# Optimization experiments

Measured on AMD Instinct MI355X. Metric: run time of the kernel, lower is better.

Reference implementation:

```python
import jax, jax.numpy as jnp
import numpy as np

B, N, Y, C = 8, 512, 64, 256


def setup_inputs() -> dict:
    key = jax.random.key(0)
    ks = jax.random.split(key, 7)
    sampled = jax.random.normal(ks[0], (B, N, Y, C), dtype=jnp.float32)
    # binary visibility mask (original passes 0/1-ish validity)
    valid = jnp.round(jax.random.uniform(ks[1], (B, N, Y), dtype=jnp.float32))
    # buffer: normalized y depth steps, y_steps = arange(Y)
    y_steps = jnp.arange(Y, dtype=jnp.float32)
    y_norm = (y_steps - y_steps.min()) / jnp.maximum(y_steps.max() - y_steps.min(), 1e-6)
    # weight_mlp = Linear(C+1 -> C), GELU, Linear(C -> 1); store weights pre-transposed (in, out)
    s1 = 1.0 / np.sqrt(C + 1)
    s2 = 1.0 / np.sqrt(C)
    W1 = jax.random.uniform(ks[2], (C + 1, C), dtype=jnp.float32, minval=-s1, maxval=s1)
    b1 = jax.random.uniform(ks[3], (C,), dtype=jnp.float32, minval=-s1, maxval=s1)
    W2 = jax.random.uniform(ks[4], (C, 1), dtype=jnp.float32, minval=-s2, maxval=s2)
    b2 = jax.random.uniform(ks[5], (1,), dtype=jnp.float32, minval=-s2, maxval=s2)
    return {"sampled": sampled, "valid": valid, "y_norm": y_norm,
            "W1": W1, "b1": b1, "W2": W2, "b2": b2}


def reference(sampled, valid, y_norm, W1, b1, W2, b2):
    b, n, y, c = sampled.shape
    yfeat = jnp.broadcast_to(y_norm.reshape(1, 1, y, 1), (b, n, y, 1))
    feat = jnp.concatenate([sampled, yfeat], axis=-1)            # [B,N,Y,C+1]
    h = jax.nn.gelu(feat @ W1 + b1, approximate=False)            # [B,N,Y,C]
    logits = (h @ W2 + b2)[..., 0]                                # [B,N,Y]
    logits = jnp.where(valid < 0.5, jnp.float32(-10000.0), logits)
    weights = jax.nn.softmax(logits, axis=-1) * valid
    denom = jnp.maximum(weights.sum(axis=-1, keepdims=True), 1e-6)
    weights = weights / denom
    return jnp.einsum('bnyc,bny->bnc', sampled, weights)          # [B,N,C]
```

## Files before the change

kernel.cpp:

```cpp
#include <hip/hip_runtime.h>

#define NTOK 4096
#define AST  264

using short8  = __attribute__((ext_vector_type(8))) short;
using short4v = __attribute__((ext_vector_type(4))) short;
using floatx4 = __attribute__((ext_vector_type(4))) float;

static __device__ __forceinline__ short f2bf(float f) {
  union { float f; unsigned u; } v; v.f = f;
  unsigned u = v.u;
  u = (u + 0x7fffu + ((u >> 16) & 1u)) >> 16;
  return (short)u;
}

static __device__ __forceinline__ float bf2f(short s) {
  union { unsigned u; float f; } v; v.u = ((unsigned)(unsigned short)s) << 16;
  return v.f;
}

static __device__ __forceinline__ float fast_gelu(float z) {
  float x  = z * 0.70710678118654752f;
  float ax = fabsf(x);
  float t  = __builtin_amdgcn_rcpf(fmaf(0.3275911f, ax, 1.0f));
  float em = __expf(-ax * ax);
  float p  = fmaf(fmaf(fmaf(fmaf(1.061405429f, t, -1.453152027f), t,
                            1.421413741f), t, -0.284496736f), t, 0.254829592f);
  float er = fmaf(-p * t, em, 1.0f);
  unsigned sgn = __float_as_uint(x) & 0x80000000u;
  er = __uint_as_float(__float_as_uint(er) | sgn);
  return z * fmaf(0.5f, er, 0.5f);
}

__global__ void prep_w1(const float* __restrict__ W1, short* __restrict__ W1s) {
  const int n  = threadIdx.x;
  const int kb = blockIdx.x;
  const int s  = kb >> 2;
  const int l  = ((kb & 3) << 4) | (n & 15);
  const int t  = n >> 4;
  short8 o;
  #pragma unroll
  for (int j = 0; j < 8; ++j)
    o[j] = f2bf(W1[(kb * 8 + j) * 256 + n]);
  *(short8*)(W1s + (((s * 16 + t) * 64 + l) << 3)) = o;
}

__global__ void __launch_bounds__(256, 4) agg_kernel(
    const float* __restrict__ sampled, const float* __restrict__ valid,
    const float* __restrict__ y_norm, const float* __restrict__ W1,
    const float* __restrict__ b1, const float* __restrict__ W2,
    const float* __restrict__ b2, const short* __restrict__ W1s,
    float* __restrict__ out) {
  __shared__ __align__(16) short Abf[64 * AST];
  __shared__ float wlog[4][64];
  __shared__ float ynl[64];

  const int tid = threadIdx.x;
  const int tok = blockIdx.x;
  const float* S = sampled + ((size_t)tok << 14);

  if (tid < 64) ynl[tid] = y_norm[tid];
  const float4* S4 = (const float4*)S;
  #pragma unroll
  for (int h = 0; h < 2; ++h) {
    float4 v[8];
    #pragma unroll
    for (int it = 0; it < 8; ++it) v[it] = S4[(h * 8 + it) * 256 + tid];
    #pragma unroll
    for (int it = 0; it < 8; ++it) {
      int j  = (h * 8 + it) * 256 + tid;
      int y  = j >> 6;
      int k4 = (j & 63) << 2;
      short4v p;
      p[0] = f2bf(v[it].x); p[1] = f2bf(v[it].y);
      p[2] = f2bf(v[it].z); p[3] = f2bf(v[it].w);
      *(short4v*)(&Abf[y * AST + k4]) = p;
    }
  }
  __syncthreads();

  const int wv  = tid >> 6;
  const int ln  = tid & 63;
  const int q   = ln >> 4;
  const int c15 = ln & 15;

  const floatx4 fzero = {0.f, 0.f, 0.f, 0.f};
  floatx4 acc[4][4];
  #pragma unroll
  for (int mt = 0; mt < 4; ++mt)
    #pragma unroll
    for (int nt = 0; nt < 4; ++nt) acc[mt][nt] = fzero;

  #pragma unroll
  for (int s = 0; s < 8; ++s) {
    short8 af[4];
    #pragma unroll
    for (int mt = 0; mt < 4; ++mt)
      af[mt] = *(const short8*)(&Abf[(mt * 16 + c15) * AST + s * 32 + q * 8]);
    #pragma unroll
    for (int nt = 0; nt < 4; ++nt) {
      const int t = wv * 4 + nt;
      short8 bfrag = *(const short8*)(W1s + (((s * 16 + t) * 64 + ln) << 3));
      #pragma unroll
      for (int mt = 0; mt < 4; ++mt)
        acc[mt][nt] = __builtin_amdgcn_mfma_f32_16x16x32_bf16(af[mt], bfrag, acc[mt][nt], 0, 0, 0);
    }
  }

  float w2v[4], b1v[4], wlv[4];
  #pragma unroll
  for (int nt = 0; nt < 4; ++nt) {
    int n = wv * 64 + nt * 16 + c15;
    w2v[nt] = W2[n];
    b1v[nt] = b1[n];
    wlv[nt] = W1[65536 + n];
  }
  #pragma unroll
  for (int mt = 0; mt < 4; ++mt) {
    #pragma unroll
    for (int r = 0; r < 4; ++r) {
      int m = mt * 16 + q * 4 + r;
      float ym = ynl[m];
      float p = 0.f;
      #pragma unroll
      for (int nt = 0; nt < 4; ++nt) {
        float z = acc[mt][nt][r] + ym * wlv[nt] + b1v[nt];
        p += fast_gelu(z) * w2v[nt];
      }
      p += __shfl_xor(p, 1);
      p += __shfl_xor(p, 2);
      p += __shfl_xor(p, 4);
      p += __shfl_xor(p, 8);
      if (c15 == 0) wlog[wv][m] = p;
    }
  }
  __syncthreads();

  float lg = wlog[0][ln] + wlog[1][ln] + wlog[2][ln] + wlog[3][ln] + b2[0];
  float vv = valid[tok * 64 + ln];
  float lm = (vv < 0.5f) ? -10000.0f : lg;
  float mx = lm;
  #pragma unroll
  for (int d = 32; d > 0; d >>= 1) mx = fmaxf(mx, __shfl_xor(mx, d));
  float e  = __expf(lm - mx);
  float s1 = e;
  #pragma unroll
  for (int d = 32; d > 0; d >>= 1) s1 += __shfl_xor(s1, d);
  float wgt = e / s1 * vv;
  float s2  = wgt;
  #pragma unroll
  for (int d = 32; d > 0; d >>= 1) s2 += __shfl_xor(s2, d);
  wgt = wgt / fmaxf(s2, 1e-6f);

  float a0 = 0.f;
  #pragma unroll
  for (int y = 0; y < 64; ++y) {
    float wy = __shfl(wgt, y);
    a0 = fmaf(bf2f(Abf[y * AST + tid]), wy, a0);
  }
  out[(size_t)tok * 256 + tid] = a0;
}

extern "C" void kernel_launch(void* const* d_in, const int* in_sizes, int n_in,
                              void* d_out, int out_size, void* d_ws, size_t ws_size,
                              hipStream_t stream) {
  const float* sampled = (const float*)d_in[0];
  const float* valid   = (const float*)d_in[1];
  const float* y_norm  = (const float*)d_in[2];
  const float* W1      = (const float*)d_in[3];
  const float* b1      = (const float*)d_in[4];
  const float* W2      = (const float*)d_in[5];
  const float* b2      = (const float*)d_in[6];
  short* W1s = (short*)d_ws;
  float* out = (float*)d_out;

  prep_w1<<<32, 256, 0, stream>>>(W1, W1s);
  agg_kernel<<<NTOK, 256, 0, stream>>>(sampled, valid, y_norm, W1, b1, W2, b2, W1s, out);
}
```

Measured before the change: 411.5 us.

## Process four tokens per block with register prefetch of next token's input

Each block now handles four tokens in a loop. The next token's sampled data is prefetched into registers while the current token's MFMA and GELU stages run, so global load latency overlaps with compute. The grid shrinks fourfold, the per-block W1/bias loads are amortized, the occupancy hint in launch bounds is dropped, and the softmax is simplified by folding the first normalization into the masked sum. The extra register pressure from the double buffer may lower occupancy, and the smaller grid may underfill the GPU.

```diff
diff --git a/kernel.cpp b/kernel.cpp
--- a/kernel.cpp
+++ b/kernel.cpp
@@ -1,6 +1,8 @@
 #include <hip/hip_runtime.h>
 
 #define NTOK 4096
+#define TPB_TOK 4
+#define GRID (NTOK / TPB_TOK)
 #define AST  264
 
 using short8  = __attribute__((ext_vector_type(8))) short;
@@ -45,7 +47,7 @@
   *(short8*)(W1s + (((s * 16 + t) * 64 + l) << 3)) = o;
 }
 
-__global__ void __launch_bounds__(256, 4) agg_kernel(
+__global__ void __launch_bounds__(256) agg_kernel(
     const float* __restrict__ sampled, const float* __restrict__ valid,
     const float* __restrict__ y_norm, const float* __restrict__ W1,
     const float* __restrict__ b1, const float* __restrict__ W2,
@@ -56,56 +58,12 @@
   __shared__ float ynl[64];
 
   const int tid = threadIdx.x;
-  const int tok = blockIdx.x;
-  const float* S = sampled + ((size_t)tok << 14);
-
-  if (tid < 64) ynl[tid] = y_norm[tid];
-  const float4* S4 = (const float4*)S;
-  #pragma unroll
-  for (int h = 0; h < 2; ++h) {
-    float4 v[8];
-    #pragma unroll
-    for (int it = 0; it < 8; ++it) v[it] = S4[(h * 8 + it) * 256 + tid];
-    #pragma unroll
-    for (int it = 0; it < 8; ++it) {
-      int j  = (h * 8 + it) * 256 + tid;
-      int y  = j >> 6;
-      int k4 = (j & 63) << 2;
-      short4v p;
-      p[0] = f2bf(v[it].x); p[1] = f2bf(v[it].y);
-      p[2] = f2bf(v[it].z); p[3] = f2bf(v[it].w);
-      *(short4v*)(&Abf[y * AST + k4]) = p;
-    }
-  }
-  __syncthreads();
-
   const int wv  = tid >> 6;
   const int ln  = tid & 63;
   const int q   = ln >> 4;
   const int c15 = ln & 15;
 
-  const floatx4 fzero = {0.f, 0.f, 0.f, 0.f};
-  floatx4 acc[4][4];
-  #pragma unroll
-  for (int mt = 0; mt < 4; ++mt)
-    #pragma unroll
-    for (int nt = 0; nt < 4; ++nt) acc[mt][nt] = fzero;
-
-  #pragma unroll
-  for (int s = 0; s < 8; ++s) {
-    short8 af[4];
-    #pragma unroll
-    for (int mt = 0; mt < 4; ++mt)
-      af[mt] = *(const short8*)(&Abf[(mt * 16 + c15) * AST + s * 32 + q * 8]);
-    #pragma unroll
-    for (int nt = 0; nt < 4; ++nt) {
-      const int t = wv * 4 + nt;
-      short8 bfrag = *(const short8*)(W1s + (((s * 16 + t) * 64 + ln) << 3));
-      #pragma unroll
-      for (int mt = 0; mt < 4; ++mt)
-        acc[mt][nt] = __builtin_amdgcn_mfma_f32_16x16x32_bf16(af[mt], bfrag, acc[mt][nt], 0, 0, 0);
-    }
-  }
+  if (tid < 64) ynl[tid] = y_norm[tid];
 
   float w2v[4], b1v[4], wlv[4];
   #pragma unroll
@@ -115,50 +73,120 @@
     b1v[nt] = b1[n];
     wlv[nt] = W1[65536 + n];
   }
-  #pragma unroll
-  for (int mt = 0; mt < 4; ++mt) {
-    #pragma unroll
-    for (int r = 0; r < 4; ++r) {
-      int m = mt * 16 + q * 4 + r;
-      float ym = ynl[m];
-      float p = 0.f;
+  const float b2s = b2[0];
+
+  const int tok0 = blockIdx.x * TPB_TOK;
+
+  float4 v0[8], v1[8];
+  float vvn;
+  {
+    const float4* S4 = (const float4*)(sampled + ((size_t)tok0 << 14));
+    #pragma unroll
+    for (int it = 0; it < 8; ++it) v0[it] = S4[it * 256 + tid];
+    #pragma unroll
+    for (int it = 0; it < 8; ++it) v1[it] = S4[(8 + it) * 256 + tid];
+    vvn = valid[tok0 * 64 + ln];
+  }
+
+  for (int t = 0; t < TPB_TOK; ++t) {
+    const int tok = tok0 + t;
+    const float4* Sn = (const float4*)(sampled + ((size_t)(tok + 1) << 14));
+
+    __syncthreads();
+
+    #pragma unroll
+    for (int it = 0; it < 8; ++it) {
+      int y = it * 4 + wv;
+      short4v p;
+      p[0] = f2bf(v0[it].x); p[1] = f2bf(v0[it].y);
+      p[2] = f2bf(v0[it].z); p[3] = f2bf(v0[it].w);
+      *(short4v*)(&Abf[y * AST + (ln << 2)]) = p;
+    }
+    #pragma unroll
+    for (int it = 0; it < 8; ++it) {
+      int y = (8 + it) * 4 + wv;
+      short4v p;
+      p[0] = f2bf(v1[it].x); p[1] = f2bf(v1[it].y);
+      p[2] = f2bf(v1[it].z); p[3] = f2bf(v1[it].w);
+      *(short4v*)(&Abf[y * AST + (ln << 2)]) = p;
+    }
+    const float vv = vvn;
+    __syncthreads();
+
+    if (t + 1 < TPB_TOK) {
+      #pragma unroll
+      for (int it = 0; it < 8; ++it) v0[it] = Sn[it * 256 + tid];
+      vvn = valid[(tok + 1) * 64 + ln];
+    }
+
+    const floatx4 fzero = {0.f, 0.f, 0.f, 0.f};
+    floatx4 acc[4][4];
+    #pragma unroll
+    for (int mt = 0; mt < 4; ++mt)
+      #pragma unroll
+      for (int nt = 0; nt < 4; ++nt) acc[mt][nt] = fzero;
+
+    #pragma unroll
+    for (int s = 0; s < 8; ++s) {
+      short8 af[4];
+      #pragma unroll
+      for (int mt = 0; mt < 4; ++mt)
+        af[mt] = *(const short8*)(&Abf[(mt * 16 + c15) * AST + s * 32 + q * 8]);
       #pragma unroll
       for (int nt = 0; nt < 4; ++nt) {
-        float z = acc[mt][nt][r] + ym * wlv[nt] + b1v[nt];
-        p += fast_gelu(z) * w2v[nt];
+        const int tt = wv * 4 + nt;
+        short8 bfrag = *(const short8*)(W1s + (((s * 16 + tt) * 64 + ln) << 3));
+        #pragma unroll
+        for (int mt = 0; mt < 4; ++mt)
+          acc[mt][nt] = __builtin_amdgcn_mfma_f32_16x16x32_bf16(af[mt], bfrag, acc[mt][nt], 0, 0, 0);
       }
-      p += __shfl_xor(p, 1);
-      p += __shfl_xor(p, 2);
-      p += __shfl_xor(p, 4);
-      p += __shfl_xor(p, 8);
-      if (c15 == 0) wlog[wv][m] = p;
-    }
+    }
+
+    if (t + 1 < TPB_TOK) {
+      #pragma unroll
+      for (int it = 0; it < 8; ++it) v1[it] = Sn[(8 + it) * 256 + tid];
+    }
+
+    #pragma unroll
+    for (int mt = 0; mt < 4; ++mt) {
+      #pragma unroll
+      for (int r = 0; r < 4; ++r) {
+        int m = mt * 16 + q * 4 + r;
+        float ym = ynl[m];
+        float p = 0.f;
+        #pragma unroll
+        for (int nt = 0; nt < 4; ++nt) {
+          float z = acc[mt][nt][r] + ym * wlv[nt] + b1v[nt];
+          p += fast_gelu(z) * w2v[nt];
+        }
+        p += __shfl_xor(p, 1);
+        p += __shfl_xor(p, 2);
+        p += __shfl_xor(p, 4);
+        p += __shfl_xor(p, 8);
+        if (c15 == 0) wlog[wv][m] = p;
+      }
+    }
+    __syncthreads();
+
+    float lg = wlog[0][ln] + wlog[1][ln] + wlog[2][ln] + wlog[3][ln] + b2s;
+    float lm = (vv < 0.5f) ? -10000.0f : lg;
+    float mx = lm;
+    #pragma unroll
+    for (int d = 32; d > 0; d >>= 1) mx = fmaxf(mx, __shfl_xor(mx, d));
+    float e   = __expf(lm - mx) * vv;
+    float s2  = e;
+    #pragma unroll
+    for (int d = 32; d > 0; d >>= 1) s2 += __shfl_xor(s2, d);
+    float wgt = e / fmaxf(s2, 1e-6f);
+
+    float a0 = 0.f;
+    #pragma unroll
+    for (int y = 0; y < 64; ++y) {
+      float wy = __shfl(wgt, y);
+      a0 = fmaf(bf2f(Abf[y * AST + tid]), wy, a0);
+    }
+    out[(size_t)tok * 256 + tid] = a0;
   }
-  __syncthreads();
-
-  float lg = wlog[0][ln] + wlog[1][ln] + wlog[2][ln] + wlog[3][ln] + b2[0];
-  float vv = valid[tok * 64 + ln];
-  float lm = (vv < 0.5f) ? -10000.0f : lg;
-  float mx = lm;
-  #pragma unroll
-  for (int d = 32; d > 0; d >>= 1) mx = fmaxf(mx, __shfl_xor(mx, d));
-  float e  = __expf(lm - mx);
-  float s1 = e;
-  #pragma unroll
-  for (int d = 32; d > 0; d >>= 1) s1 += __shfl_xor(s1, d);
-  float wgt = e / s1 * vv;
-  float s2  = wgt;
-  #pragma unroll
-  for (int d = 32; d > 0; d >>= 1) s2 += __shfl_xor(s2, d);
-  wgt = wgt / fmaxf(s2, 1e-6f);
-
-  float a0 = 0.f;
-  #pragma unroll
-  for (int y = 0; y < 64; ++y) {
-    float wy = __shfl(wgt, y);
-    a0 = fmaf(bf2f(Abf[y * AST + tid]), wy, a0);
-  }
-  out[(size_t)tok * 256 + tid] = a0;
 }
 
 extern "C" void kernel_launch(void* const* d_in, const int* in_sizes, int n_in,
@@ -175,5 +203,5 @@
   float* out = (float*)d_out;
 
   prep_w1<<<32, 256, 0, stream>>>(W1, W1s);
-  agg_kernel<<<NTOK, 256, 0, stream>>>(sampled, valid, y_norm, W1, b1, W2, b2, W1s, out);
-}
+  agg_kernel<<<GRID, 256, 0, stream>>>(sampled, valid, y_norm, W1, b1, W2, b2, W1s, out);
+}
```

After: 451.1 us. +9.6%, slower.

## Split token GEMM across eight waves with prefetched B fragments

Applied to the files above, without the earlier changes.

Doubles the block to 512 threads so each of eight waves computes two 16-column N tiles instead of four, which halves accumulator registers per wave and adds more waves for latency hiding. Weight fragments for the next K step are prefetched into registers, and the bf16 conversion uses the packed HIP intrinsic. Bias and weight loads are hoisted above the GEMM. The softmax drops one reduction by folding normalization into the masked sum, and waves 4-7 exit early. The trade-off is more per-block synchronization and work duplication for the per-row logit reduction across eight partial sums.

```diff
diff --git a/kernel.cpp b/kernel.cpp
--- a/kernel.cpp
+++ b/kernel.cpp
@@ -1,10 +1,10 @@
 #include <hip/hip_runtime.h>
+#include <hip/hip_bf16.h>
 
 #define NTOK 4096
 #define AST  264
 
 using short8  = __attribute__((ext_vector_type(8))) short;
-using short4v = __attribute__((ext_vector_type(4))) short;
 using floatx4 = __attribute__((ext_vector_type(4))) float;
 
 static __device__ __forceinline__ short f2bf(float f) {
@@ -17,6 +17,12 @@
 static __device__ __forceinline__ float bf2f(short s) {
   union { unsigned u; float f; } v; v.u = ((unsigned)(unsigned short)s) << 16;
   return v.f;
+}
+
+static __device__ __forceinline__ unsigned pack_bf2(float a, float b) {
+  __hip_bfloat162 h = __float22bfloat162_rn(float2{a, b});
+  union { __hip_bfloat162 h; unsigned u; } v; v.h = h;
+  return v.u;
 }
 
 static __device__ __forceinline__ float fast_gelu(float z) {
@@ -45,76 +51,85 @@
   *(short8*)(W1s + (((s * 16 + t) * 64 + l) << 3)) = o;
 }
 
-__global__ void __launch_bounds__(256, 4) agg_kernel(
+__global__ void __launch_bounds__(512, 4) agg_kernel(
     const float* __restrict__ sampled, const float* __restrict__ valid,
     const float* __restrict__ y_norm, const float* __restrict__ W1,
     const float* __restrict__ b1, const float* __restrict__ W2,
     const float* __restrict__ b2, const short* __restrict__ W1s,
     float* __restrict__ out) {
   __shared__ __align__(16) short Abf[64 * AST];
-  __shared__ float wlog[4][64];
+  __shared__ float wlog[8][64];
   __shared__ float ynl[64];
 
   const int tid = threadIdx.x;
+  const int wv  = tid >> 6;
+  const int ln  = tid & 63;
+  const int q   = ln >> 4;
+  const int c15 = ln & 15;
   const int tok = blockIdx.x;
+
   const float* S = sampled + ((size_t)tok << 14);
+  if (tid < 64) ynl[tid] = y_norm[tid];
+  const float vv = valid[tok * 64 + ln];
 
-  if (tid < 64) ynl[tid] = y_norm[tid];
-  const float4* S4 = (const float4*)S;
+  float w2v[2], b1v[2], wlv[2];
   #pragma unroll
-  for (int h = 0; h < 2; ++h) {
+  for (int nt = 0; nt < 2; ++nt) {
+    int n = (wv * 2 + nt) * 16 + c15;
+    w2v[nt] = W2[n];
+    b1v[nt] = b1[n];
+    wlv[nt] = W1[65536 + n];
+  }
+  const float b2s = b2[0];
+
+  {
+    const float4* S4 = (const float4*)S;
     float4 v[8];
     #pragma unroll
-    for (int it = 0; it < 8; ++it) v[it] = S4[(h * 8 + it) * 256 + tid];
+    for (int it = 0; it < 8; ++it) v[it] = S4[it * 512 + tid];
     #pragma unroll
     for (int it = 0; it < 8; ++it) {
-      int j  = (h * 8 + it) * 256 + tid;
+      int j  = it * 512 + tid;
       int y  = j >> 6;
       int k4 = (j & 63) << 2;
-      short4v p;
-      p[0] = f2bf(v[it].x); p[1] = f2bf(v[it].y);
-      p[2] = f2bf(v[it].z); p[3] = f2bf(v[it].w);
-      *(short4v*)(&Abf[y * AST + k4]) = p;
+      uint2 p;
+      p.x = pack_bf2(v[it].x, v[it].y);
+      p.y = pack_bf2(v[it].z, v[it].w);
+      *(uint2*)(&Abf[y * AST + k4]) = p;
     }
   }
   __syncthreads();
 
-  const int wv  = tid >> 6;
-  const int ln  = tid & 63;
-  const int q   = ln >> 4;
-  const int c15 = ln & 15;
+  const short8* Wq = (const short8*)W1s;
+  const int tb = wv * 2;
 
   const floatx4 fzero = {0.f, 0.f, 0.f, 0.f};
-  floatx4 acc[4][4];
+  floatx4 acc[4][2];
   #pragma unroll
-  for (int mt = 0; mt < 4; ++mt)
-    #pragma unroll
-    for (int nt = 0; nt < 4; ++nt) acc[mt][nt] = fzero;
+  for (int mt = 0; mt < 4; ++mt) { acc[mt][0] = fzero; acc[mt][1] = fzero; }
 
+  short8 bc0 = Wq[(0 * 16 + tb + 0) * 64 + ln];
+  short8 bc1 = Wq[(0 * 16 + tb + 1) * 64 + ln];
   #pragma unroll
   for (int s = 0; s < 8; ++s) {
+    short8 bn0, bn1;
+    if (s < 7) {
+      bn0 = Wq[((s + 1) * 16 + tb + 0) * 64 + ln];
+      bn1 = Wq[((s + 1) * 16 + tb + 1) * 64 + ln];
+    }
     short8 af[4];
     #pragma unroll
     for (int mt = 0; mt < 4; ++mt)
       af[mt] = *(const short8*)(&Abf[(mt * 16 + c15) * AST + s * 32 + q * 8]);
     #pragma unroll
-    for (int nt = 0; nt < 4; ++nt) {
-      const int t = wv * 4 + nt;
-      short8 bfrag = *(const short8*)(W1s + (((s * 16 + t) * 64 + ln) << 3));
-      #pragma unroll
-      for (int mt = 0; mt < 4; ++mt)
-        acc[mt][nt] = __builtin_amdgcn_mfma_f32_16x16x32_bf16(af[mt], bfrag, acc[mt][nt], 0, 0, 0);
-    }
+    for (int mt = 0; mt < 4; ++mt)
+      acc[mt][0] = __builtin_amdgcn_mfma_f32_16x16x32_bf16(af[mt], bc0, acc[mt][0], 0, 0, 0);
+    #pragma unroll
+    for (int mt = 0; mt < 4; ++mt)
+      acc[mt][1] = __builtin_amdgcn_mfma_f32_16x16x32_bf16(af[mt], bc1, acc[mt][1], 0, 0, 0);
+    bc0 = bn0; bc1 = bn1;
   }
 
-  float w2v[4], b1v[4], wlv[4];
-  #pragma unroll
-  for (int nt = 0; nt < 4; ++nt) {
-    int n = wv * 64 + nt * 16 + c15;
-    w2v[nt] = W2[n];
-    b1v[nt] = b1[n];
-    wlv[nt] = W1[65536 + n];
-  }
   #pragma unroll
   for (int mt = 0; mt < 4; ++mt) {
     #pragma unroll
@@ -123,7 +138,7 @@
       float ym = ynl[m];
       float p = 0.f;
       #pragma unroll
-      for (int nt = 0; nt < 4; ++nt) {
+      for (int nt = 0; nt < 2; ++nt) {
         float z = acc[mt][nt][r] + ym * wlv[nt] + b1v[nt];
         p += fast_gelu(z) * w2v[nt];
       }
@@ -136,21 +151,20 @@
   }
   __syncthreads();
 
-  float lg = wlog[0][ln] + wlog[1][ln] + wlog[2][ln] + wlog[3][ln] + b2[0];
-  float vv = valid[tok * 64 + ln];
+  if (wv >= 4) return;
+
+  float lg = b2s;
+  #pragma unroll
+  for (int w = 0; w < 8; ++w) lg += wlog[w][ln];
   float lm = (vv < 0.5f) ? -10000.0f : lg;
   float mx = lm;
   #pragma unroll
   for (int d = 32; d > 0; d >>= 1) mx = fmaxf(mx, __shfl_xor(mx, d));
-  float e  = __expf(lm - mx);
-  float s1 = e;
-  #pragma unroll
-  for (int d = 32; d > 0; d >>= 1) s1 += __shfl_xor(s1, d);
-  float wgt = e / s1 * vv;
-  float s2  = wgt;
+  float e  = __expf(lm - mx) * vv;
+  float s2 = e;
   #pragma unroll
   for (int d = 32; d > 0; d >>= 1) s2 += __shfl_xor(s2, d);
-  wgt = wgt / fmaxf(s2, 1e-6f);
+  float wgt = e / fmaxf(s2, 1e-6f);
 
   float a0 = 0.f;
   #pragma unroll
@@ -175,5 +189,5 @@
   float* out = (float*)d_out;
 
   prep_w1<<<32, 256, 0, stream>>>(W1, W1s);
-  agg_kernel<<<NTOK, 256, 0, stream>>>(sampled, valid, y_norm, W1, b1, W2, b2, W1s, out);
+  agg_kernel<<<NTOK, 512, 0, stream>>>(sampled, valid, y_norm, W1, b1, W2, b2, W1s, out);
 }
```

After: 418.1 us. No clear change (+1.6%).
